# Optimization experiments

Hardware: AMD Instinct MI355X
Metric: run time of the kernel (lower is better)

Reference implementation:

```python
import jax, jax.numpy as jnp
import numpy as np

EPS = 1e-5

def _conv1(x, W):
    # 1x1 conv: W [Cout, Cin], x [B, Cin, H, W]
    return jnp.einsum('oi,bihw->bohw', W, x)

def _bn(x, p):
    # p: [4, C] rows = (gamma, beta, running_mean, running_var); inference-mode BN
    g, b, m, v = p[0], p[1], p[2], p[3]
    s = (1, -1, 1, 1)
    return (x - m.reshape(s)) * (g.reshape(s) * jax.lax.rsqrt(v.reshape(s) + EPS)) + b.reshape(s)

def _block(x, W1, p1, W2, p2):
    # Conv1x1 -> BN -> ReLU -> Conv1x1 -> BN -> ReLU  (Composition / Decomposition conv block)
    h = jax.nn.relu(_bn(_conv1(x, W1), p1))
    return jax.nn.relu(_bn(_conv1(h, W2), p2))

def _gru(h, x, Wg, bg, Wc, bc):
    # ConvGRU cell with 1x1 kernels: h is prev hidden, x is message input
    g = jax.nn.sigmoid(_conv1(jnp.concatenate([x, h], axis=1), Wg) + bg.reshape(1, -1, 1, 1))
    r, u = jnp.split(g, 2, axis=1)  # reset, update gates
    c = jnp.tanh(_conv1(jnp.concatenate([x, r * h], axis=1), Wc) + bc.reshape(1, -1, 1, 1))
    return (1.0 - u) * h + u * c


def setup_inputs() -> dict:
    key = jax.random.key(0)
    B, HD, H, W = 8, 10, 192, 192
    ks = iter(jax.random.split(key, 64))
    def nrm(shape, s=1.0):
        return s * jax.random.normal(next(ks), shape, dtype=jnp.float32)
    def att(shape):
        return jax.random.uniform(next(ks), shape, dtype=jnp.float32)
    def bnp(C):
        return jnp.stack([
            jax.random.uniform(next(ks), (C,), minval=0.5, maxval=1.5, dtype=jnp.float32),
            0.1 * jax.random.normal(next(ks), (C,), dtype=jnp.float32),
            0.1 * jax.random.normal(next(ks), (C,), dtype=jnp.float32),
            jax.random.uniform(next(ks), (C,), minval=0.5, maxval=1.5, dtype=jnp.float32)])
    inp = dict(
        xf=nrm((B, HD, H, W)),
        xh=nrm((2, B, HD, H, W)),
        xp=nrm((6, B, HD, H, W)),
        h_att=att((3, B, 1, H, W)),
        p_att=att((7, B, 1, H, W)),
        dW1=nrm((2 * HD, 2 * HD), 0.2), dbn1=bnp(2 * HD), dW2=nrm((HD, 2 * HD), 0.2), dbn2=bnp(HD),
        uW1=nrm((2 * HD, 2 * HD), 0.2), ubn1=bnp(2 * HD), uW2=nrm((HD, 2 * HD), 0.2), ubn2=bnp(HD),
        lW1=nrm((2 * HD, 2 * HD), 0.2), lbn1=bnp(2 * HD), lW2=nrm((HD, 2 * HD), 0.2), lbn2=bnp(HD),
        guWg=nrm((2 * HD, 2 * HD), 0.2), gubg=nrm((2 * HD,), 0.1),
        guWc=nrm((HD, 2 * HD), 0.2), gubc=nrm((HD,), 0.1),
        glWg=nrm((2 * HD, 2 * HD), 0.2), glbg=nrm((2 * HD,), 0.1),
        glWc=nrm((HD, 2 * HD), 0.2), glbc=nrm((HD,), 0.1),
    )
    return inp


def reference(xf, xh, xp, h_att, p_att,
              dW1, dbn1, dW2, dbn2,
              uW1, ubn1, uW2, ubn2,
              lW1, lbn1, lW2, lbn2,
              guWg, gubg, guWc, gubc,
              glWg, glbg, glWc, glbc):
    # Decomposition: conv_fh(cat(xf * h_att[i+1], xh[i])) for the two halves
    decomp_u = _block(jnp.concatenate([xf * h_att[1], xh[0]], axis=1), dW1, dbn1, dW2, dbn2)
    decomp_l = _block(jnp.concatenate([xf * h_att[2], xh[1]], axis=1), dW1, dbn1, dW2, dbn2)
    # Composition upper: parts 1..4 -> xp[0..3], attention maps p_att[1..4]
    com_att_u = p_att[1] + p_att[2] + p_att[3] + p_att[4]
    comp_u = sum(_block(jnp.concatenate([xh[0], xp[i] * com_att_u], axis=1), uW1, ubn1, uW2, ubn2)
                 for i in range(4))
    xh_u = _gru(xh[0], decomp_u + comp_u, guWg, gubg, guWc, gubc)
    # Composition lower: parts 5..6 -> xp[4..5], attention maps p_att[5..6]
    com_att_l = p_att[5] + p_att[6]
    comp_l = sum(_block(jnp.concatenate([xh[1], xp[i] * com_att_l], axis=1), lW1, lbn1, lW2, lbn2)
                 for i in (4, 5))
    xh_l = _gru(xh[1], decomp_l + comp_l, glWg, glbg, glWc, glbc)
    return jnp.stack([xh_u, xh_l])  # [2, B, hidden, H, W]
```

## Files before the change

kernel.cpp:

```cpp
#include <hip/hip_runtime.h>

#define HD 10
#define C2 20
#define PIX (192*192)
#define NB 8
#define NPIX (NB*PIX)
#define CHW (NB*HD*PIX)
#define EPSB 1e-5f

__device__ __forceinline__ float sigm(float x) {
    return __builtin_amdgcn_rcpf(1.0f + __expf(-x));
}
__device__ __forceinline__ float tanh_fast(float x) {
    return 1.0f - 2.0f * __builtin_amdgcn_rcpf(1.0f + __expf(2.0f * x));
}

__global__ __launch_bounds__(256) void half_kernel(
    const float* __restrict__ xf, const float* __restrict__ xh, const float* __restrict__ xp,
    const float* __restrict__ h_att, const float* __restrict__ p_att,
    const float* __restrict__ dW1, const float* __restrict__ dbn1,
    const float* __restrict__ dW2, const float* __restrict__ dbn2,
    const float* __restrict__ uW1, const float* __restrict__ ubn1,
    const float* __restrict__ uW2, const float* __restrict__ ubn2,
    const float* __restrict__ lW1, const float* __restrict__ lbn1,
    const float* __restrict__ lW2, const float* __restrict__ lbn2,
    const float* __restrict__ guWg, const float* __restrict__ gubg,
    const float* __restrict__ guWc, const float* __restrict__ gubc,
    const float* __restrict__ glWg, const float* __restrict__ glbg,
    const float* __restrict__ glWc, const float* __restrict__ glbc,
    float* __restrict__ out)
{
    const int half = blockIdx.y;
    const int t = blockIdx.x * 256 + threadIdx.x;
    const int b = t / PIX;
    const int s = t - b * PIX;
    const int base  = b * (HD*PIX) + s;
    const int abase = b * PIX + s;

    const float* Wc1  = half ? lW1  : uW1;
    const float* cbn1 = half ? lbn1 : ubn1;
    const float* Wc2  = half ? lW2  : uW2;
    const float* cbn2 = half ? lbn2 : ubn2;
    const float* Wg = half ? glWg : guWg;
    const float* bg = half ? glbg : gubg;
    const float* Wc = half ? glWc : guWc;
    const float* bc = half ? glbc : gubc;

    const float* xhh = xh + half * CHW;
    float* outh = out + half * CHW;

    float vxh[HD];
    #pragma unroll
    for (int c = 0; c < HD; ++c) vxh[c] = xhh[base + c*PIX];

    const float ha = h_att[(1 + half) * NPIX + abase];
    float catt = 0.f;
    {
        const int mstart = half ? 5 : 1;
        const int natt   = half ? 2 : 4;
        for (int j = 0; j < natt; ++j) catt += p_att[(mstart + j) * NPIX + abase];
    }

    float m[HD];
    {
        float in[C2];
        #pragma unroll
        for (int c = 0; c < HD; ++c) { in[c] = xf[base + c*PIX] * ha; in[HD + c] = vxh[c]; }
        float h[C2];
        #pragma unroll
        for (int o = 0; o < C2; ++o) {
            float a = 0.f;
            #pragma unroll
            for (int k = 0; k < C2; ++k) a = fmaf(dW1[o*C2 + k], in[k], a);
            float sc = dbn1[o] * rsqrtf(dbn1[3*C2 + o] + EPSB);
            float tr = dbn1[C2 + o] - sc * dbn1[2*C2 + o];
            h[o] = fmaxf(fmaf(a, sc, tr), 0.f);
        }
        #pragma unroll
        for (int o = 0; o < HD; ++o) {
            float a = 0.f;
            #pragma unroll
            for (int k = 0; k < C2; ++k) a = fmaf(dW2[o*C2 + k], h[k], a);
            float sc = dbn2[o] * rsqrtf(dbn2[3*HD + o] + EPSB);
            float tr = dbn2[HD + o] - sc * dbn2[2*HD + o];
            m[o] = fmaxf(fmaf(a, sc, tr), 0.f);
        }
    }

    {
        float s1[C2], s2[HD], t2[HD];
        #pragma unroll
        for (int o = 0; o < C2; ++o)
            s1[o] = cbn1[o] * rsqrtf(cbn1[3*C2 + o] + EPSB);
        #pragma unroll
        for (int o = 0; o < HD; ++o) {
            s2[o] = cbn2[o] * rsqrtf(cbn2[3*HD + o] + EPSB);
            t2[o] = cbn2[HD + o] - s2[o] * cbn2[2*HD + o];
        }
        float pre[C2];
        #pragma unroll
        for (int o = 0; o < C2; ++o) {
            float a = 0.f;
            #pragma unroll
            for (int k = 0; k < HD; ++k) a = fmaf(Wc1[o*C2 + k], vxh[k], a);
            float t1 = cbn1[C2 + o] - s1[o] * cbn1[2*C2 + o];
            pre[o] = fmaf(a, s1[o], t1);
        }
        const int pstart = half ? 4 : 0;
        const int nparts = half ? 2 : 4;
        for (int i = 0; i < nparts; ++i) {
            float xpi[HD];
            #pragma unroll
            for (int c = 0; c < HD; ++c)
                xpi[c] = xp[(pstart + i) * CHW + base + c*PIX] * catt;
            float h[C2];
            #pragma unroll
            for (int o = 0; o < C2; ++o) {
                float a = 0.f;
                #pragma unroll
                for (int k = 0; k < HD; ++k) a = fmaf(Wc1[o*C2 + HD + k], xpi[k], a);
                h[o] = fmaxf(fmaf(a, s1[o], pre[o]), 0.f);
            }
            #pragma unroll
            for (int o = 0; o < HD; ++o) {
                float a = 0.f;
                #pragma unroll
                for (int k = 0; k < C2; ++k) a = fmaf(Wc2[o*C2 + k], h[k], a);
                m[o] += fmaxf(fmaf(a, s2[o], t2[o]), 0.f);
            }
        }
    }

    float g[C2];
    #pragma unroll
    for (int o = 0; o < C2; ++o) {
        float a = bg[o];
        #pragma unroll
        for (int k = 0; k < HD; ++k) a = fmaf(Wg[o*C2 + k], m[k], a);
        #pragma unroll
        for (int k = 0; k < HD; ++k) a = fmaf(Wg[o*C2 + HD + k], vxh[k], a);
        g[o] = sigm(a);
    }
    float rh[HD];
    #pragma unroll
    for (int k = 0; k < HD; ++k) rh[k] = g[k] * vxh[k];
    #pragma unroll
    for (int o = 0; o < HD; ++o) {
        float a = bc[o];
        #pragma unroll
        for (int k = 0; k < HD; ++k) a = fmaf(Wc[o*C2 + k], m[k], a);
        #pragma unroll
        for (int k = 0; k < HD; ++k) a = fmaf(Wc[o*C2 + HD + k], rh[k], a);
        float c = tanh_fast(a);
        float u = g[HD + o];
        outh[base + o*PIX] = fmaf(u, c - vxh[o], vxh[o]);
    }
}

extern "C" void kernel_launch(void* const* d_in, const int* in_sizes, int n_in,
                              void* d_out, int out_size, void* d_ws, size_t ws_size,
                              hipStream_t stream) {
    const float* xf    = (const float*)d_in[0];
    const float* xh    = (const float*)d_in[1];
    const float* xp    = (const float*)d_in[2];
    const float* h_att = (const float*)d_in[3];
    const float* p_att = (const float*)d_in[4];
    const float* dW1   = (const float*)d_in[5];
    const float* dbn1  = (const float*)d_in[6];
    const float* dW2   = (const float*)d_in[7];
    const float* dbn2  = (const float*)d_in[8];
    const float* uW1   = (const float*)d_in[9];
    const float* ubn1  = (const float*)d_in[10];
    const float* uW2   = (const float*)d_in[11];
    const float* ubn2  = (const float*)d_in[12];
    const float* lW1   = (const float*)d_in[13];
    const float* lbn1  = (const float*)d_in[14];
    const float* lW2   = (const float*)d_in[15];
    const float* lbn2  = (const float*)d_in[16];
    const float* guWg  = (const float*)d_in[17];
    const float* gubg  = (const float*)d_in[18];
    const float* guWc  = (const float*)d_in[19];
    const float* gubc  = (const float*)d_in[20];
    const float* glWg  = (const float*)d_in[21];
    const float* glbg  = (const float*)d_in[22];
    const float* glWc  = (const float*)d_in[23];
    const float* glbc  = (const float*)d_in[24];

    dim3 grid(NPIX / 256, 2), block(256);
    half_kernel<<<grid, block, 0, stream>>>(
        xf, xh, xp, h_att, p_att,
        dW1, dbn1, dW2, dbn2,
        uW1, ubn1, uW2, ubn2,
        lW1, lbn1, lW2, lbn2,
        guWg, gubg, guWc, gubc,
        glWg, glbg, glWc, glbc,
        (float*)d_out);
}
```

Baseline: 117.8 us.

## Process two pixels per thread with float2 loads and interleave halves in blocks

Each thread now handles two adjacent pixels, using float2 vector loads and stores, so every scalar weight load is reused for two FMAs. The grid is flattened and the upper and lower halves are interleaved across consecutive block IDs, so blocks that read the same xf and attention data run close together and share cache. Launch bounds now ask for 3 blocks per SIMD unit to limit register use. The cost is doubled register arrays per thread, which may cause spills under the tighter register cap.

```diff
diff --git a/kernel.cpp b/kernel.cpp
--- a/kernel.cpp
+++ b/kernel.cpp
@@ -7,6 +7,8 @@
 #define NPIX (NB*PIX)
 #define CHW (NB*HD*PIX)
 #define EPSB 1e-5f
+#define PXB 512
+#define BPB (PIX/PXB)
 
 __device__ __forceinline__ float sigm(float x) {
     return __builtin_amdgcn_rcpf(1.0f + __expf(-x));
@@ -15,7 +17,7 @@
     return 1.0f - 2.0f * __builtin_amdgcn_rcpf(1.0f + __expf(2.0f * x));
 }
 
-__global__ __launch_bounds__(256) void half_kernel(
+__global__ __launch_bounds__(256, 3) void half_kernel(
     const float* __restrict__ xf, const float* __restrict__ xh, const float* __restrict__ xp,
     const float* __restrict__ h_att, const float* __restrict__ p_att,
     const float* __restrict__ dW1, const float* __restrict__ dbn1,
@@ -30,10 +32,11 @@
     const float* __restrict__ glWc, const float* __restrict__ glbc,
     float* __restrict__ out)
 {
-    const int half = blockIdx.y;
-    const int t = blockIdx.x * 256 + threadIdx.x;
-    const int b = t / PIX;
-    const int s = t - b * PIX;
+    const int bid  = blockIdx.x;
+    const int half = bid & 1;
+    const int bx   = bid >> 1;
+    const int b    = bx / BPB;
+    const int s    = (bx - b * BPB) * PXB + threadIdx.x * 2;
     const int base  = b * (HD*PIX) + s;
     const int abase = b * PIX + s;
 
@@ -49,41 +52,63 @@
     const float* xhh = xh + half * CHW;
     float* outh = out + half * CHW;
 
-    float vxh[HD];
-    #pragma unroll
-    for (int c = 0; c < HD; ++c) vxh[c] = xhh[base + c*PIX];
-
-    const float ha = h_att[(1 + half) * NPIX + abase];
-    float catt = 0.f;
+#define LD2(p, off) (*reinterpret_cast<const float2*>((p) + (off)))
+
+    float vxhx[HD], vxhy[HD];
+    #pragma unroll
+    for (int c = 0; c < HD; ++c) {
+        float2 v = LD2(xhh, base + c*PIX);
+        vxhx[c] = v.x; vxhy[c] = v.y;
+    }
+
+    const float2 hav = LD2(h_att, (1 + half) * NPIX + abase);
+    float cax = 0.f, cay = 0.f;
     {
         const int mstart = half ? 5 : 1;
         const int natt   = half ? 2 : 4;
-        for (int j = 0; j < natt; ++j) catt += p_att[(mstart + j) * NPIX + abase];
-    }
-
-    float m[HD];
+        for (int j = 0; j < natt; ++j) {
+            float2 v = LD2(p_att, (mstart + j) * NPIX + abase);
+            cax += v.x; cay += v.y;
+        }
+    }
+
+    float mx[HD], my[HD];
     {
-        float in[C2];
-        #pragma unroll
-        for (int c = 0; c < HD; ++c) { in[c] = xf[base + c*PIX] * ha; in[HD + c] = vxh[c]; }
-        float h[C2];
+        float inx[C2], iny[C2];
+        #pragma unroll
+        for (int c = 0; c < HD; ++c) {
+            float2 v = LD2(xf, base + c*PIX);
+            inx[c] = v.x * hav.x;  iny[c] = v.y * hav.y;
+            inx[HD + c] = vxhx[c]; iny[HD + c] = vxhy[c];
+        }
+        float h0x[C2], h0y[C2];
         #pragma unroll
         for (int o = 0; o < C2; ++o) {
-            float a = 0.f;
-            #pragma unroll
-            for (int k = 0; k < C2; ++k) a = fmaf(dW1[o*C2 + k], in[k], a);
+            float ax = 0.f, ay = 0.f;
+            #pragma unroll
+            for (int k = 0; k < C2; ++k) {
+                float w = dW1[o*C2 + k];
+                ax = fmaf(w, inx[k], ax);
+                ay = fmaf(w, iny[k], ay);
+            }
             float sc = dbn1[o] * rsqrtf(dbn1[3*C2 + o] + EPSB);
             float tr = dbn1[C2 + o] - sc * dbn1[2*C2 + o];
-            h[o] = fmaxf(fmaf(a, sc, tr), 0.f);
+            h0x[o] = fmaxf(fmaf(ax, sc, tr), 0.f);
+            h0y[o] = fmaxf(fmaf(ay, sc, tr), 0.f);
         }
         #pragma unroll
         for (int o = 0; o < HD; ++o) {
-            float a = 0.f;
-            #pragma unroll
-            for (int k = 0; k < C2; ++k) a = fmaf(dW2[o*C2 + k], h[k], a);
+            float ax = 0.f, ay = 0.f;
+            #pragma unroll
+            for (int k = 0; k < C2; ++k) {
+                float w = dW2[o*C2 + k];
+                ax = fmaf(w, h0x[k], ax);
+                ay = fmaf(w, h0y[k], ay);
+            }
             float sc = dbn2[o] * rsqrtf(dbn2[3*HD + o] + EPSB);
             float tr = dbn2[HD + o] - sc * dbn2[2*HD + o];
-            m[o] = fmaxf(fmaf(a, sc, tr), 0.f);
+            mx[o] = fmaxf(fmaf(ax, sc, tr), 0.f);
+            my[o] = fmaxf(fmaf(ay, sc, tr), 0.f);
         }
     }
 
@@ -97,64 +122,104 @@
             s2[o] = cbn2[o] * rsqrtf(cbn2[3*HD + o] + EPSB);
             t2[o] = cbn2[HD + o] - s2[o] * cbn2[2*HD + o];
         }
-        float pre[C2];
+        float prex[C2], prey[C2];
         #pragma unroll
         for (int o = 0; o < C2; ++o) {
-            float a = 0.f;
-            #pragma unroll
-            for (int k = 0; k < HD; ++k) a = fmaf(Wc1[o*C2 + k], vxh[k], a);
+            float ax = 0.f, ay = 0.f;
+            #pragma unroll
+            for (int k = 0; k < HD; ++k) {
+                float w = Wc1[o*C2 + k];
+                ax = fmaf(w, vxhx[k], ax);
+                ay = fmaf(w, vxhy[k], ay);
+            }
             float t1 = cbn1[C2 + o] - s1[o] * cbn1[2*C2 + o];
-            pre[o] = fmaf(a, s1[o], t1);
+            prex[o] = fmaf(ax, s1[o], t1);
+            prey[o] = fmaf(ay, s1[o], t1);
         }
         const int pstart = half ? 4 : 0;
         const int nparts = half ? 2 : 4;
         for (int i = 0; i < nparts; ++i) {
-            float xpi[HD];
-            #pragma unroll
-            for (int c = 0; c < HD; ++c)
-                xpi[c] = xp[(pstart + i) * CHW + base + c*PIX] * catt;
-            float h[C2];
+            float xpx[HD], xpy[HD];
+            #pragma unroll
+            for (int c = 0; c < HD; ++c) {
+                float2 v = LD2(xp, (pstart + i) * CHW + base + c*PIX);
+                xpx[c] = v.x * cax; xpy[c] = v.y * cay;
+            }
+            float hx[C2], hy[C2];
             #pragma unroll
             for (int o = 0; o < C2; ++o) {
-                float a = 0.f;
+                float ax = 0.f, ay = 0.f;
                 #pragma unroll
-                for (int k = 0; k < HD; ++k) a = fmaf(Wc1[o*C2 + HD + k], xpi[k], a);
-                h[o] = fmaxf(fmaf(a, s1[o], pre[o]), 0.f);
+                for (int k = 0; k < HD; ++k) {
+                    float w = Wc1[o*C2 + HD + k];
+                    ax = fmaf(w, xpx[k], ax);
+                    ay = fmaf(w, xpy[k], ay);
+                }
+                hx[o] = fmaxf(fmaf(ax, s1[o], prex[o]), 0.f);
+                hy[o] = fmaxf(fmaf(ay, s1[o], prey[o]), 0.f);
             }
             #pragma unroll
             for (int o = 0; o < HD; ++o) {
-                float a = 0.f;
+                float ax = 0.f, ay = 0.f;
                 #pragma unroll
-                for (int k = 0; k < C2; ++k) a = fmaf(Wc2[o*C2 + k], h[k], a);
-                m[o] += fmaxf(fmaf(a, s2[o], t2[o]), 0.f);
-            }
-        }
-    }
-
-    float g[C2];
+                for (int k = 0; k < C2; ++k) {
+                    float w = Wc2[o*C2 + k];
+                    ax = fmaf(w, hx[k], ax);
+                    ay = fmaf(w, hy[k], ay);
+                }
+                mx[o] += fmaxf(fmaf(ax, s2[o], t2[o]), 0.f);
+                my[o] += fmaxf(fmaf(ay, s2[o], t2[o]), 0.f);
+            }
+        }
+    }
+
+    float gx[C2], gy[C2];
     #pragma unroll
     for (int o = 0; o < C2; ++o) {
-        float a = bg[o];
-        #pragma unroll
-        for (int k = 0; k < HD; ++k) a = fmaf(Wg[o*C2 + k], m[k], a);
-        #pragma unroll
-        for (int k = 0; k < HD; ++k) a = fmaf(Wg[o*C2 + HD + k], vxh[k], a);
-        g[o] = sigm(a);
-    }
-    float rh[HD];
-    #pragma unroll
-    for (int k = 0; k < HD; ++k) rh[k] = g[k] * vxh[k];
+        float ax = bg[o], ay = ax;
+        #pragma unroll
+        for (int k = 0; k < HD; ++k) {
+            float w = Wg[o*C2 + k];
+            ax = fmaf(w, mx[k], ax);
+            ay = fmaf(w, my[k], ay);
+        }
+        #pragma unroll
+        for (int k = 0; k < HD; ++k) {
+            float w = Wg[o*C2 + HD + k];
+            ax = fmaf(w, vxhx[k], ax);
+            ay = fmaf(w, vxhy[k], ay);
+        }
+        gx[o] = sigm(ax);
+        gy[o] = sigm(ay);
+    }
+    float rhx[HD], rhy[HD];
+    #pragma unroll
+    for (int k = 0; k < HD; ++k) {
+        rhx[k] = gx[k] * vxhx[k];
+        rhy[k] = gy[k] * vxhy[k];
+    }
     #pragma unroll
     for (int o = 0; o < HD; ++o) {
-        float a = bc[o];
-        #pragma unroll
-        for (int k = 0; k < HD; ++k) a = fmaf(Wc[o*C2 + k], m[k], a);
-        #pragma unroll
-        for (int k = 0; k < HD; ++k) a = fmaf(Wc[o*C2 + HD + k], rh[k], a);
-        float c = tanh_fast(a);
-        float u = g[HD + o];
-        outh[base + o*PIX] = fmaf(u, c - vxh[o], vxh[o]);
-    }
+        float ax = bc[o], ay = ax;
+        #pragma unroll
+        for (int k = 0; k < HD; ++k) {
+            float w = Wc[o*C2 + k];
+            ax = fmaf(w, mx[k], ax);
+            ay = fmaf(w, my[k], ay);
+        }
+        #pragma unroll
+        for (int k = 0; k < HD; ++k) {
+            float w = Wc[o*C2 + HD + k];
+            ax = fmaf(w, rhx[k], ax);
+            ay = fmaf(w, rhy[k], ay);
+        }
+        float cxv = tanh_fast(ax), cyv = tanh_fast(ay);
+        float2 o2;
+        o2.x = fmaf(gx[HD + o], cxv - vxhx[o], vxhx[o]);
+        o2.y = fmaf(gy[HD + o], cyv - vxhy[o], vxhy[o]);
+        *reinterpret_cast<float2*>(outh + base + o*PIX) = o2;
+    }
+#undef LD2
 }
 
 extern "C" void kernel_launch(void* const* d_in, const int* in_sizes, int n_in,
@@ -186,7 +251,7 @@
     const float* glWc  = (const float*)d_in[23];
     const float* glbc  = (const float*)d_in[24];
 
-    dim3 grid(NPIX / 256, 2), block(256);
+    dim3 grid((NPIX / PXB) * 2), block(256);
     half_kernel<<<grid, block, 0, stream>>>(
         xf, xh, xp, h_att, p_att,
         dW1, dbn1, dW2, dbn2,
```

New measurement: 160.9 us. +36.6%, slower.
